# Kernel tuning notes

Measured on AMD Instinct MI355X. Metric: run time of the kernel, lower is better.

The kernel has to match this reference:

```python
import jax, jax.numpy as jnp
import numpy as np

HS = [192, 96, 48, 24, 12, 6]
WS = [384, 192, 96, 48, 24, 12]
C = 64    # feature channels per pyramid level
F = 64    # num_features (conv output channels)
CIN = 2 * C + 2  # current + warped + 2 flow channels = 130
N = 4


def dense_image_warp(image, flow):
    """tfa.image.dense_image_warp: warped[b,y,x] = bilinear(image[b, y - flow_y, x - flow_x]).
    Boundary handling matches tfa._interpolate_bilinear: floor indices clipped to
    [0, size-2], interpolation alphas clipped to [0, 1]."""
    n, h, w, _ = image.shape
    gy, gx = jnp.meshgrid(jnp.arange(h, dtype=flow.dtype),
                          jnp.arange(w, dtype=flow.dtype), indexing='ij')
    qy = gy[None] - flow[..., 0]          # [N,H,W] query rows
    qx = gx[None] - flow[..., 1]          # [N,H,W] query cols
    y0 = jnp.clip(jnp.floor(qy), 0, h - 2).astype(jnp.int32)
    x0 = jnp.clip(jnp.floor(qx), 0, w - 2).astype(jnp.int32)
    ay = jnp.clip(qy - y0.astype(flow.dtype), 0.0, 1.0)[..., None]
    ax = jnp.clip(qx - x0.astype(flow.dtype), 0.0, 1.0)[..., None]
    b = jnp.arange(n)[:, None, None]
    tl = image[b, y0, x0]
    tr = image[b, y0, x0 + 1]
    bl = image[b, y0 + 1, x0]
    br = image[b, y0 + 1, x0 + 1]
    top = tl + (tr - tl) * ax
    bot = bl + (br - bl) * ax
    return top + (bot - top) * ay


def separable_conv1x1(x, dw, pw, bias):
    # SeparableConv2D with 1x1 kernel: depthwise per-channel scale, then pointwise matmul.
    return jnp.einsum('nhwc,cf->nhwf', x * dw, pw) + bias


def _forward(xcs, xps, fls, dws, pws, bs):
    outs = []
    for i in range(6):
        # _warp: dense_image_warp(x_prev, -flow)
        warped = dense_image_warp(xps[i], -fls[i])
        x = jnp.concatenate([xcs[i], warped, fls[i]], axis=-1)  # [N,H,W,130]
        outs.append(separable_conv1x1(x, dws[i], pws[i], bs[i]))
    return tuple(outs)


def setup_inputs() -> dict:
    key = jax.random.key(0)
    d = {}
    for i in range(6):
        h, w = HS[i], WS[i]
        ks = jax.random.split(jax.random.fold_in(key, i), 6)
        d[f'xc{i}'] = jax.random.normal(ks[0], (N, h, w, C), jnp.float32)
        d[f'xp{i}'] = jax.random.normal(ks[1], (N, h, w, C), jnp.float32)
        d[f'fl{i}'] = jax.random.normal(ks[2], (N, h, w, 2), jnp.float32) * 2.0
        d[f'dw{i}'] = jax.random.normal(ks[3], (CIN,), jnp.float32) * 0.1
        d[f'pw{i}'] = jax.random.normal(ks[4], (CIN, F), jnp.float32) * 0.05
        d[f'bias{i}'] = jnp.zeros((F,), jnp.float32)
    return d


def reference(xc0, xc1, xc2, xc3, xc4, xc5,
              xp0, xp1, xp2, xp3, xp4, xp5,
              fl0, fl1, fl2, fl3, fl4, fl5,
              dw0, dw1, dw2, dw3, dw4, dw5,
              pw0, pw1, pw2, pw3, pw4, pw5,
              bias0, bias1, bias2, bias3, bias4, bias5):
    xcs = (xc0, xc1, xc2, xc3, xc4, xc5)
    xps = (xp0, xp1, xp2, xp3, xp4, xp5)
    fls = (fl0, fl1, fl2, fl3, fl4, fl5)
    dws = (dw0, dw1, dw2, dw3, dw4, dw5)
    pws = (pw0, pw1, pw2, pw3, pw4, pw5)
    bs = (bias0, bias1, bias2, bias3, bias4, bias5)
    return _forward(xcs, xps, fls, dws, pws, bs)
```

## Files before the change

kernel.cpp:

```cpp
#include <hip/hip_runtime.h>


typedef __attribute__((ext_vector_type(8))) short bf16x8;
typedef __attribute__((ext_vector_type(4))) float f32x4;

#define WS_LVL_STRIDE 17408

__device__ inline unsigned rne_bf16_bits(float f) {
  unsigned u = __builtin_bit_cast(unsigned, f);
  u += 0x7fffu + ((u >> 16) & 1u);
  return u >> 16;
}
__device__ inline int pack_bf16x2(float a, float b) {
  return (int)(rne_bf16_bits(a) | (rne_bf16_bits(b) << 16));
}

struct LevelArgs {
  const float* __restrict__ xc;
  const float* __restrict__ xp;
  const float* __restrict__ fl;
  float* __restrict__ out;
  const char* __restrict__ wsl;
  int H, W, npix, block_start;
};
struct KArgs { LevelArgs lv[6]; int total_blocks; };

struct PrepLevel {
  const float* __restrict__ dw;
  const float* __restrict__ pw;
  const float* __restrict__ bias;
  char* __restrict__ wsl;
};
struct PrepArgs { PrepLevel lv[6]; };

__global__ void prep_kernel(PrepArgs pa) {
  const PrepLevel P = pa.lv[blockIdx.x];
  int4* __restrict__ frag = (int4*)P.wsl;
  for (int e = (int)threadIdx.x; e < 1024; e += 256) {
    const int kt = e >> 8;
    const int nt = (e >> 6) & 3;
    const int lane = e & 63;
    const int n = 4 * (lane & 15) + nt;
    const int kb = kt * 32 + ((lane >> 4) & 3) * 8;
    int v[4];
#pragma unroll
    for (int jj = 0; jj < 4; ++jj) {
      const int k0 = kb + jj * 2;
      const float w0 = P.dw[k0] * P.pw[(size_t)k0 * 64 + n];
      const float w1 = P.dw[k0 + 1] * P.pw[(size_t)(k0 + 1) * 64 + n];
      v[jj] = pack_bf16x2(w0, w1);
    }
    frag[e] = make_int4(v[0], v[1], v[2], v[3]);
  }
  float* __restrict__ tab = (float*)(P.wsl + 16384);
  if (threadIdx.x < 64) {
    const int f = (int)threadIdx.x;
    tab[f] = P.bias[f];
    tab[64 + f] = P.dw[128] * P.pw[128 * 64 + f];
    tab[128 + f] = P.dw[129] * P.pw[129 * 64 + f];
  }
}

#define SWZ(r, o) \
  ((((unsigned)(r)) << 7) | (((unsigned)(o)) ^ ((((unsigned)(r)) & 7u) << 4)))

__global__ __launch_bounds__(256, 5) void flowwarp_mfma(KArgs ka) {
  __shared__ __align__(16) char lds_raw[256 * 128];

  const int nb = ka.total_blocks;
  const int chunk = (nb + 7) >> 3;
  const int bp = (int)blockIdx.x;
  const int b = (bp & 7) * chunk + (bp >> 3);
  if (b >= nb) return;

  int Lr = 0;
#pragma unroll
  for (int i = 1; i < 6; ++i) Lr = (b >= ka.lv[i].block_start) ? i : Lr;
  const int L = __builtin_amdgcn_readfirstlane(Lr);
  const LevelArgs A = ka.lv[L];

  const int q = (int)threadIdx.x;
  const int p0 = (b - A.block_start) * 256;
  const int W = A.W, H = A.H;
  const int lane = q & 63;
  const int w = q >> 6;
  const int wbase = w * 64;

  float fl0, fl1;

  {
    int p = p0 + q;
    if (p > A.npix - 1) p = A.npix - 1;
    const int x = p % W;
    const int t = p / W;
    const int y = t % H;
    const int n = t / H;

    fl0 = A.fl[2 * (size_t)p];
    fl1 = A.fl[2 * (size_t)p + 1];

    const float qy = (float)y + fl0;
    const float qx = (float)x + fl1;
    const float fy = fminf(fmaxf(floorf(qy), 0.0f), (float)(H - 2));
    const float fx = fminf(fmaxf(floorf(qx), 0.0f), (float)(W - 2));
    const int y0 = (int)fy, x0 = (int)fx;
    const float ay = fminf(fmaxf(qy - fy, 0.0f), 1.0f);
    const float ax = fminf(fmaxf(qx - fx, 0.0f), 1.0f);
    const unsigned off = (unsigned)((n * H + y0) * W + x0) * 256u;

    const char* __restrict__ xpb = (const char*)A.xp;
    const int W256 = W * 256;
    const int g = lane >> 2;
    const int s16 = (lane & 3) * 16;

#pragma unroll 1
    for (int r = 0; r < 4; ++r) {
      const int src = r * 16 + g;
      const unsigned offB = (unsigned)__shfl((int)off, src);
      const float axB = __shfl(ax, src);
      const float ayB = __shfl(ay, src);
      const int lrow = wbase + src;

#pragma unroll
      for (int h = 0; h < 2; ++h) {
        f32x4 ctl[2], ctr[2], cbl[2], cbr[2];
#pragma unroll
        for (int qd = 0; qd < 2; ++qd) {
          const int o = (h * 2 + qd) * 64 + s16;
          ctl[qd] = *(const f32x4*)(xpb + offB + o);
          ctr[qd] = *(const f32x4*)(xpb + offB + 256 + o);
          cbl[qd] = *(const f32x4*)(xpb + offB + W256 + o);
          cbr[qd] = *(const f32x4*)(xpb + offB + W256 + 256 + o);
        }
#pragma unroll
        for (int qd = 0; qd < 2; ++qd) {
          float wv[4];
#pragma unroll
          for (int j = 0; j < 4; ++j) {
            const float top = fmaf(ctr[qd][j] - ctl[qd][j], axB, ctl[qd][j]);
            const float bot = fmaf(cbr[qd][j] - cbl[qd][j], axB, cbl[qd][j]);
            wv[j] = fmaf(bot - top, ayB, top);
          }
          const int ob = (h * 2 + qd) * 32 + (lane & 3) * 8;
          *(int2*)(lds_raw + SWZ(lrow, ob)) =
              make_int2(pack_bf16x2(wv[0], wv[1]), pack_bf16x2(wv[2], wv[3]));
        }
      }
    }
  }
  asm volatile("s_waitcnt lgkmcnt(0)" ::: "memory");

  const int m16 = lane & 15;
  const int q4l = lane >> 4;

  const int4* __restrict__ bfr = (const int4*)A.wsl;
  bf16x8 Bf[4][4];
#pragma unroll
  for (int kt = 0; kt < 4; ++kt)
#pragma unroll
    for (int nt = 0; nt < 4; ++nt)
      Bf[kt][nt] = __builtin_bit_cast(bf16x8, bfr[(kt * 4 + nt) * 64 + lane]);

  const float* __restrict__ tab = (const float*)(A.wsl + 16384);
  const f32x4 bvv  = *(const f32x4*)(tab + 4 * m16);
  const f32x4 t0vv = *(const f32x4*)(tab + 64 + 4 * m16);
  const f32x4 t1vv = *(const f32x4*)(tab + 128 + 4 * m16);

  const int npix1 = A.npix - 1;
  int pm = p0 + wbase + m16;
  if (pm > npix1) pm = npix1;
  const float* __restrict__ xcp = A.xc + (size_t)pm * 64 + q4l * 8;
  f32x4 na0 = *(const f32x4*)xcp;
  f32x4 na1 = *(const f32x4*)(xcp + 4);
  f32x4 na2 = *(const f32x4*)(xcp + 32);
  f32x4 na3 = *(const f32x4*)(xcp + 36);

#pragma unroll 1
  for (int mt = 0; mt < 4; ++mt) {
    const int lrow = wbase + mt * 16;
    const f32x4 a0 = na0, a1 = na1, a2 = na2, a3 = na3;
    if (mt < 3) {
      int pn = p0 + lrow + 16 + m16;
      if (pn > npix1) pn = npix1;
      const float* __restrict__ xn = A.xc + (size_t)pn * 64 + q4l * 8;
      na0 = *(const f32x4*)xn;
      na1 = *(const f32x4*)(xn + 4);
      na2 = *(const f32x4*)(xn + 32);
      na3 = *(const f32x4*)(xn + 36);
    }
    int av[8];
    av[0] = pack_bf16x2(a0[0], a0[1]); av[1] = pack_bf16x2(a0[2], a0[3]);
    av[2] = pack_bf16x2(a1[0], a1[1]); av[3] = pack_bf16x2(a1[2], a1[3]);
    av[4] = pack_bf16x2(a2[0], a2[1]); av[5] = pack_bf16x2(a2[2], a2[3]);
    av[6] = pack_bf16x2(a3[0], a3[1]); av[7] = pack_bf16x2(a3[2], a3[3]);
    const bf16x8 A0 = __builtin_bit_cast(bf16x8, make_int4(av[0], av[1], av[2], av[3]));
    const bf16x8 A1 = __builtin_bit_cast(bf16x8, make_int4(av[4], av[5], av[6], av[7]));
    const int rr = lrow + m16;
    const bf16x8 A2 = __builtin_bit_cast(
        bf16x8, *(const int4*)(lds_raw + SWZ(rr, q4l * 16)));
    const bf16x8 A3 = __builtin_bit_cast(
        bf16x8, *(const int4*)(lds_raw + SWZ(rr, 64 + q4l * 16)));

    f32x4 acc[4] = {{0.f, 0.f, 0.f, 0.f}, {0.f, 0.f, 0.f, 0.f},
                    {0.f, 0.f, 0.f, 0.f}, {0.f, 0.f, 0.f, 0.f}};
#pragma unroll
    for (int nt = 0; nt < 4; ++nt) {
      acc[nt] = __builtin_amdgcn_mfma_f32_16x16x32_bf16(A0, Bf[0][nt], acc[nt], 0, 0, 0);
      acc[nt] = __builtin_amdgcn_mfma_f32_16x16x32_bf16(A1, Bf[1][nt], acc[nt], 0, 0, 0);
      acc[nt] = __builtin_amdgcn_mfma_f32_16x16x32_bf16(A2, Bf[2][nt], acc[nt], 0, 0, 0);
      acc[nt] = __builtin_amdgcn_mfma_f32_16x16x32_bf16(A3, Bf[3][nt], acc[nt], 0, 0, 0);
    }

#pragma unroll
    for (int i = 0; i < 4; ++i) {
      const int srcl = mt * 16 + q4l * 4 + i;
      const float f0i = __shfl(fl0, srcl);
      const float f1i = __shfl(fl1, srcl);
      const int prow = p0 + lrow + q4l * 4 + i;
      if (prow < A.npix) {
        f32x4 o;
        o[0] = acc[0][i] + bvv[0] + f0i * t0vv[0] + f1i * t1vv[0];
        o[1] = acc[1][i] + bvv[1] + f0i * t0vv[1] + f1i * t1vv[1];
        o[2] = acc[2][i] + bvv[2] + f0i * t0vv[2] + f1i * t1vv[2];
        o[3] = acc[3][i] + bvv[3] + f0i * t0vv[3] + f1i * t1vv[3];
        *(f32x4*)(A.out + (size_t)prow * 64 + 4 * m16) = o;
      }
    }
  }
}

extern "C" void kernel_launch(void* const* d_in, const int* in_sizes, int n_in,
                              void* d_out, int out_size, void* d_ws, size_t ws_size,
                              hipStream_t stream) {
  static const int HS[6] = {192, 96, 48, 24, 12, 6};
  static const int WS[6] = {384, 192, 96, 48, 24, 12};
  PrepArgs pa;
  KArgs ka;
  int bstart = 0;
  size_t ooff = 0;
  for (int i = 0; i < 6; ++i) {
    char* wsl = (char*)d_ws + (size_t)i * WS_LVL_STRIDE;
    pa.lv[i].dw   = (const float*)d_in[6 * i + 3];
    pa.lv[i].pw   = (const float*)d_in[6 * i + 4];
    pa.lv[i].bias = (const float*)d_in[6 * i + 5];
    pa.lv[i].wsl  = wsl;
    ka.lv[i].xc  = (const float*)d_in[6 * i + 0];
    ka.lv[i].xp  = (const float*)d_in[6 * i + 1];
    ka.lv[i].fl  = (const float*)d_in[6 * i + 2];
    ka.lv[i].out = (float*)d_out + ooff;
    ka.lv[i].wsl = wsl;
    const int npix = 4 * HS[i] * WS[i];
    ka.lv[i].H = HS[i];
    ka.lv[i].W = WS[i];
    ka.lv[i].npix = npix;
    ka.lv[i].block_start = bstart;
    bstart += (npix + 255) / 256;
    ooff += (size_t)npix * 64;
  }
  ka.total_blocks = bstart;
  prep_kernel<<<dim3(6), dim3(256), 0, stream>>>(pa);
  const int chunk = (bstart + 7) >> 3;
  flowwarp_mfma<<<dim3(chunk * 8), dim3(256), 0, stream>>>(ka);
}
```

Before: 375.4 us.

## Pre-convert previous-frame features to fp16 for half-width bilinear gathers

Adds a conversion kernel that writes every level's xp tensor into workspace as fp16. The fused warp+MFMA kernel then gathers the four bilinear corners from this half-size copy, using 16-byte fp16 loads per corner. The aim is to halve the bytes moved by the scattered gathers and cut the number of load instructions. In exchange it adds a full extra read of xp plus a write pass, and fp16 rounding of the inputs. The new path is taken only when the workspace is large enough, otherwise it falls back to fp32.

```diff
diff --git a/kernel.cpp b/kernel.cpp
--- a/kernel.cpp
+++ b/kernel.cpp
@@ -3,8 +3,10 @@
 
 typedef __attribute__((ext_vector_type(8))) short bf16x8;
 typedef __attribute__((ext_vector_type(4))) float f32x4;
+typedef __attribute__((ext_vector_type(8))) _Float16 f16x8;
 
 #define WS_LVL_STRIDE 17408
+#define XPC_OFF (6 * WS_LVL_STRIDE)
 
 __device__ inline unsigned rne_bf16_bits(float f) {
   unsigned u = __builtin_bit_cast(unsigned, f);
@@ -21,6 +23,7 @@
   const float* __restrict__ fl;
   float* __restrict__ out;
   const char* __restrict__ wsl;
+  const char* __restrict__ xph;
   int H, W, npix, block_start;
 };
 struct KArgs { LevelArgs lv[6]; int total_blocks; };
@@ -32,6 +35,30 @@
   char* __restrict__ wsl;
 };
 struct PrepArgs { PrepLevel lv[6]; };
+
+struct CvtArgs {
+  const float* __restrict__ src[6];
+  char* __restrict__ dst;
+  int start[6];
+};
+
+__global__ void cvt_kernel(CvtArgs ca) {
+  const int i8 = (int)(blockIdx.x * 256 + threadIdx.x);
+  const int e = i8 * 8;
+  int l = 0;
+#pragma unroll
+  for (int i = 1; i < 6; ++i) l = (e >= ca.start[i]) ? i : l;
+  const float* __restrict__ s = ca.src[l] + (e - ca.start[l]);
+  const f32x4 a = *(const f32x4*)s;
+  const f32x4 b = *(const f32x4*)(s + 4);
+  f16x8 o;
+#pragma unroll
+  for (int j = 0; j < 4; ++j) {
+    o[j] = (_Float16)a[j];
+    o[4 + j] = (_Float16)b[j];
+  }
+  *(f16x8*)(ca.dst + (size_t)e * 2) = o;
+}
 
 __global__ void prep_kernel(PrepArgs pa) {
   const PrepLevel P = pa.lv[blockIdx.x];
@@ -106,44 +133,88 @@
     const int y0 = (int)fy, x0 = (int)fx;
     const float ay = fminf(fmaxf(qy - fy, 0.0f), 1.0f);
     const float ax = fminf(fmaxf(qx - fx, 0.0f), 1.0f);
-    const unsigned off = (unsigned)((n * H + y0) * W + x0) * 256u;
-
-    const char* __restrict__ xpb = (const char*)A.xp;
-    const int W256 = W * 256;
+    const int offIdx = (n * H + y0) * W + x0;
+
     const int g = lane >> 2;
-    const int s16 = (lane & 3) * 16;
-
+    const int s = lane & 3;
+
+    if (A.xph) {
+      const char* __restrict__ xpb = A.xph;
+      const int W128 = W * 128;
+      const unsigned offh = (unsigned)offIdx * 128u;
 #pragma unroll 1
-    for (int r = 0; r < 4; ++r) {
-      const int src = r * 16 + g;
-      const unsigned offB = (unsigned)__shfl((int)off, src);
-      const float axB = __shfl(ax, src);
-      const float ayB = __shfl(ay, src);
-      const int lrow = wbase + src;
-
-#pragma unroll
-      for (int h = 0; h < 2; ++h) {
-        f32x4 ctl[2], ctr[2], cbl[2], cbr[2];
-#pragma unroll
-        for (int qd = 0; qd < 2; ++qd) {
-          const int o = (h * 2 + qd) * 64 + s16;
-          ctl[qd] = *(const f32x4*)(xpb + offB + o);
-          ctr[qd] = *(const f32x4*)(xpb + offB + 256 + o);
-          cbl[qd] = *(const f32x4*)(xpb + offB + W256 + o);
-          cbr[qd] = *(const f32x4*)(xpb + offB + W256 + 256 + o);
+      for (int r = 0; r < 4; ++r) {
+        const int src = r * 16 + g;
+        const unsigned offB = (unsigned)__shfl((int)offh, src);
+        const float axB = __shfl(ax, src);
+        const float ayB = __shfl(ay, src);
+        const int lrow = wbase + src;
+        f16x8 ctl[2], ctr[2], cbl[2], cbr[2];
+#pragma unroll
+        for (int h = 0; h < 2; ++h) {
+          const int o = h * 64 + s * 16;
+          ctl[h] = *(const f16x8*)(xpb + offB + o);
+          ctr[h] = *(const f16x8*)(xpb + offB + 128 + o);
+          cbl[h] = *(const f16x8*)(xpb + offB + W128 + o);
+          cbr[h] = *(const f16x8*)(xpb + offB + W128 + 128 + o);
         }
 #pragma unroll
-        for (int qd = 0; qd < 2; ++qd) {
-          float wv[4];
-#pragma unroll
-          for (int j = 0; j < 4; ++j) {
-            const float top = fmaf(ctr[qd][j] - ctl[qd][j], axB, ctl[qd][j]);
-            const float bot = fmaf(cbr[qd][j] - cbl[qd][j], axB, cbl[qd][j]);
-            wv[j] = fmaf(bot - top, ayB, top);
+        for (int h = 0; h < 2; ++h) {
+          int v[4];
+#pragma unroll
+          for (int jj = 0; jj < 4; ++jj) {
+            float wv[2];
+#pragma unroll
+            for (int k = 0; k < 2; ++k) {
+              const int j = jj * 2 + k;
+              const float ftl = (float)ctl[h][j], ftr = (float)ctr[h][j];
+              const float fbl = (float)cbl[h][j], fbr = (float)cbr[h][j];
+              const float top = fmaf(ftr - ftl, axB, ftl);
+              const float bot = fmaf(fbr - fbl, axB, fbl);
+              wv[k] = fmaf(bot - top, ayB, top);
+            }
+            v[jj] = pack_bf16x2(wv[0], wv[1]);
           }
-          const int ob = (h * 2 + qd) * 32 + (lane & 3) * 8;
-          *(int2*)(lds_raw + SWZ(lrow, ob)) =
-              make_int2(pack_bf16x2(wv[0], wv[1]), pack_bf16x2(wv[2], wv[3]));
+          *(int4*)(lds_raw + SWZ(lrow, h * 64 + s * 16)) =
+              make_int4(v[0], v[1], v[2], v[3]);
+        }
+      }
+    } else {
+      const char* __restrict__ xpb = (const char*)A.xp;
+      const int W256 = W * 256;
+      const unsigned off = (unsigned)offIdx * 256u;
+      const int s16 = s * 16;
+#pragma unroll 1
+      for (int r = 0; r < 4; ++r) {
+        const int src = r * 16 + g;
+        const unsigned offB = (unsigned)__shfl((int)off, src);
+        const float axB = __shfl(ax, src);
+        const float ayB = __shfl(ay, src);
+        const int lrow = wbase + src;
+#pragma unroll
+        for (int h = 0; h < 2; ++h) {
+          f32x4 ctl[2], ctr[2], cbl[2], cbr[2];
+#pragma unroll
+          for (int qd = 0; qd < 2; ++qd) {
+            const int o = (h * 2 + qd) * 64 + s16;
+            ctl[qd] = *(const f32x4*)(xpb + offB + o);
+            ctr[qd] = *(const f32x4*)(xpb + offB + 256 + o);
+            cbl[qd] = *(const f32x4*)(xpb + offB + W256 + o);
+            cbr[qd] = *(const f32x4*)(xpb + offB + W256 + 256 + o);
+          }
+#pragma unroll
+          for (int qd = 0; qd < 2; ++qd) {
+            float wv[4];
+#pragma unroll
+            for (int j = 0; j < 4; ++j) {
+              const float top = fmaf(ctr[qd][j] - ctl[qd][j], axB, ctl[qd][j]);
+              const float bot = fmaf(cbr[qd][j] - cbl[qd][j], axB, cbl[qd][j]);
+              wv[j] = fmaf(bot - top, ayB, top);
+            }
+            const int ob = (h * 2 + qd) * 32 + s * 8;
+            *(int2*)(lds_raw + SWZ(lrow, ob)) =
+                make_int2(pack_bf16x2(wv[0], wv[1]), pack_bf16x2(wv[2], wv[3]));
+          }
         }
       }
     }
@@ -236,19 +307,34 @@
   static const int WS[6] = {384, 192, 96, 48, 24, 12};
   PrepArgs pa;
   KArgs ka;
+  CvtArgs ca;
   int bstart = 0;
   size_t ooff = 0;
+  int estart = 0;
+  int estarts[6];
+  for (int i = 0; i < 6; ++i) {
+    const int npix = 4 * HS[i] * WS[i];
+    estarts[i] = estart;
+    estart += npix * 64;
+  }
+  const size_t xpc_bytes = (size_t)estart * 2;
+  const bool usef16 = ws_size >= (size_t)XPC_OFF + xpc_bytes;
+  char* xpc = (char*)d_ws + XPC_OFF;
+
   for (int i = 0; i < 6; ++i) {
     char* wsl = (char*)d_ws + (size_t)i * WS_LVL_STRIDE;
     pa.lv[i].dw   = (const float*)d_in[6 * i + 3];
     pa.lv[i].pw   = (const float*)d_in[6 * i + 4];
     pa.lv[i].bias = (const float*)d_in[6 * i + 5];
     pa.lv[i].wsl  = wsl;
+    ca.src[i]     = (const float*)d_in[6 * i + 1];
+    ca.start[i]   = estarts[i];
     ka.lv[i].xc  = (const float*)d_in[6 * i + 0];
     ka.lv[i].xp  = (const float*)d_in[6 * i + 1];
     ka.lv[i].fl  = (const float*)d_in[6 * i + 2];
     ka.lv[i].out = (float*)d_out + ooff;
     ka.lv[i].wsl = wsl;
+    ka.lv[i].xph = usef16 ? (xpc + (size_t)estarts[i] * 2) : nullptr;
     const int npix = 4 * HS[i] * WS[i];
     ka.lv[i].H = HS[i];
     ka.lv[i].W = WS[i];
@@ -258,7 +344,13 @@
     ooff += (size_t)npix * 64;
   }
   ka.total_blocks = bstart;
+  ca.dst = xpc;
+
   prep_kernel<<<dim3(6), dim3(256), 0, stream>>>(pa);
+  if (usef16) {
+    const int cvt_blocks = estart / 8 / 256;
+    cvt_kernel<<<dim3(cvt_blocks), dim3(256), 0, stream>>>(ca);
+  }
   const int chunk = (bstart + 7) >> 3;
   flowwarp_mfma<<<dim3(chunk * 8), dim3(256), 0, stream>>>(ka);
 }
```

Result: no change. 382.6 us (+1.9%).
